# Kernel optimization log

Measured on AMD Instinct MI355X. Metric: run time of the kernel, lower is better.

## Reference

```python
import jax, jax.numpy as jnp
import numpy as np

D = 1024
H = 16
B = 4
L = 1024
EPS = 1e-5


def _ln(x, g, b):
    m = jnp.mean(x, axis=-1, keepdims=True)
    v = jnp.mean((x - m) ** 2, axis=-1, keepdims=True)
    return (x - m) / jnp.sqrt(v + EPS) * g + b


def _bn_eval(x, g, b, mean, var):
    # x: [B, L, C]; per-channel batchnorm in eval mode
    return (x - mean) / jnp.sqrt(var + EPS) * g + b


def setup_inputs() -> dict:
    key = jax.random.key(0)
    ks = jax.random.split(key, 16)
    s = 0.02
    return {
        "q": jax.random.normal(ks[0], (B, L, D), jnp.float32),
        "wq": jax.random.normal(ks[1], (D, D), jnp.float32) * s,
        "bq": jax.random.normal(ks[2], (D,), jnp.float32) * s,
        "wk": jax.random.normal(ks[3], (D, D), jnp.float32) * s,
        "bk": jax.random.normal(ks[4], (D,), jnp.float32) * s,
        "wv": jax.random.normal(ks[5], (D, D), jnp.float32) * s,
        "bv": jax.random.normal(ks[6], (D,), jnp.float32) * s,
        "wo": jax.random.normal(ks[7], (D, D), jnp.float32) * s,
        "bo": jax.random.normal(ks[8], (D,), jnp.float32) * s,
        "w1": jax.random.normal(ks[9], (4 * D, D), jnp.float32) * s,
        "bn1_g": jax.random.uniform(ks[10], (4 * D,), jnp.float32, 0.5, 1.5),
        "bn1_b": jax.random.normal(ks[11], (4 * D,), jnp.float32) * s,
        "bn1_m": jax.random.normal(ks[12], (4 * D,), jnp.float32) * s,
        "bn1_v": jax.random.uniform(ks[13], (4 * D,), jnp.float32, 0.5, 1.5),
        "w2": jax.random.normal(ks[14], (D, 4 * D), jnp.float32) * s,
        "bn2_g": jax.random.uniform(ks[15], (D,), jnp.float32, 0.5, 1.5),
        "bn2_b": jnp.zeros((D,), jnp.float32),
        "bn2_m": jnp.zeros((D,), jnp.float32),
        "bn2_v": jnp.ones((D,), jnp.float32),
        "ln1_g": jnp.ones((D,), jnp.float32),
        "ln1_b": jnp.zeros((D,), jnp.float32),
        "ln3_g": jnp.ones((D,), jnp.float32),
        "ln3_b": jnp.zeros((D,), jnp.float32),
    }


def reference(q, wq, bq, wk, bk, wv, bv, wo, bo,
              w1, bn1_g, bn1_b, bn1_m, bn1_v,
              w2, bn2_g, bn2_b, bn2_m, bn2_v,
              ln1_g, ln1_b, ln3_g, ln3_b):
    hd = D // H
    scale = hd ** -0.5
    # conv1x1 projections == per-token linear: [B,L,D] @ [D,D]^T + bias
    qp = (q @ wq.T + bq).reshape(B, L, H, hd)
    kp = (q @ wk.T + bk).reshape(B, L, H, hd)
    vp = (q @ wv.T + bv).reshape(B, L, H, hd)
    attn = jnp.einsum('blhd,bmhd->bhlm', qp, kp) * scale  # [B,H,L,L]
    attn = jax.nn.softmax(attn, axis=-1)
    out = jnp.einsum('bhlm,bmhd->blhd', attn, vp).reshape(B, L, D)
    out = out @ wo.T + bo
    # post-norm residual block (norm_first=False, use_residual=True)
    x = _ln(q + out, ln1_g, ln1_b)
    # conv-MLP: 1x1 conv -> BN(eval) -> GELU(exact) -> 1x1 conv -> BN(eval)
    h = x @ w1.T                                   # [B,L,4D]
    h = jax.nn.gelu(_bn_eval(h, bn1_g, bn1_b, bn1_m, bn1_v), approximate=False)
    h = _bn_eval(h @ w2.T, bn2_g, bn2_b, bn2_m, bn2_v)  # [B,L,D]
    x = _ln(x + h, ln3_g, ln3_b)
    return x
```

## Files before the change

### kernel.cpp

```cpp
#include <hip/hip_runtime.h>
#include <math.h>

#define EPS 1e-5f

typedef unsigned short ushort_t;
typedef __attribute__((ext_vector_type(8))) __bf16 bf16x8;
typedef __attribute__((ext_vector_type(4))) __bf16 bf16x4;
typedef __attribute__((ext_vector_type(4))) float f32x4;

#define MFMA16(a, b, c) __builtin_amdgcn_mfma_f32_16x16x32_bf16(a, b, c, 0, 0, 0)

#define QSCALE2 0.18033688011112042f

__device__ __forceinline__ unsigned short f2bf(float f) {
  unsigned u = __float_as_uint(f);
  u += 0x7fffu + ((u >> 16) & 1u);
  return (unsigned short)(u >> 16);
}

__device__ __forceinline__ void gload16(const void* g, void* l) {
  __builtin_amdgcn_global_load_lds(
      (__attribute__((address_space(1))) void*)(g),
      (__attribute__((address_space(3))) void*)(l), 16, 0, 0);
}

__global__ __launch_bounds__(256) void cast_all_k(
    const float* __restrict__ wq, const float* __restrict__ wk,
    const float* __restrict__ wv, const float* __restrict__ wo,
    const float* __restrict__ w1, const float* __restrict__ w2,
    const float* __restrict__ q, ushort_t* __restrict__ wqkv,
    ushort_t* __restrict__ wob, ushort_t* __restrict__ w1b,
    ushort_t* __restrict__ w2b, ushort_t* __restrict__ qbf) {
  const int b = blockIdx.x;
  const float* src;
  ushort_t* dst;
  int idx;
  if (b < 2048) {
    const int s = b >> 9;
    src = (s == 0) ? wq : (s == 1) ? wk : (s == 2) ? wv : wo;
    dst = (s == 3) ? wob : wqkv + s * 1048576;
    idx = (b & 511) * 2048 + threadIdx.x * 8;
  } else if (b < 4096) {
    src = w1; dst = w1b; idx = (b - 2048) * 2048 + threadIdx.x * 8;
  } else if (b < 6144) {
    src = w2; dst = w2b; idx = (b - 4096) * 2048 + threadIdx.x * 8;
  } else {
    src = q; dst = qbf; idx = (b - 6144) * 2048 + threadIdx.x * 8;
  }
  float4 a = *(const float4*)(src + idx);
  float4 c = *(const float4*)(src + idx + 4);
  uint4 u;
  u.x = (unsigned)f2bf(a.x) | ((unsigned)f2bf(a.y) << 16);
  u.y = (unsigned)f2bf(a.z) | ((unsigned)f2bf(a.w) << 16);
  u.z = (unsigned)f2bf(c.x) | ((unsigned)f2bf(c.y) << 16);
  u.w = (unsigned)f2bf(c.z) | ((unsigned)f2bf(c.w) << 16);
  *(uint4*)(dst + idx) = u;
}

__global__ __launch_bounds__(256) void bnparam_k(
    const float* __restrict__ g1, const float* __restrict__ b1,
    const float* __restrict__ m1, const float* __restrict__ v1,
    const float* __restrict__ g2, const float* __restrict__ b2,
    const float* __restrict__ m2, const float* __restrict__ v2,
    float* __restrict__ sc1, float* __restrict__ sh1,
    float* __restrict__ sc2, float* __restrict__ sh2) {
  int i = blockIdx.x * 256 + threadIdx.x;
  if (i < 4096) {
    float s = g1[i] * rsqrtf(v1[i] + EPS);
    sc1[i] = s;
    sh1[i] = b1[i] - m1[i] * s;
  } else if (i < 5120) {
    int j = i - 4096;
    float s = g2[j] * rsqrtf(v2[j] + EPS);
    sc2[j] = s;
    sh2[j] = b2[j] - m2[j] * s;
  }
}

template <int KDIM, int EPI, int TM, int TN, int GX, int GY>
__global__ __launch_bounds__(256) void gemm_bt(const ushort_t* __restrict__ A,
                                               const ushort_t* __restrict__ W,
                                               const float* __restrict__ p0,
                                               const float* __restrict__ p1,
                                               const float* __restrict__ p2,
                                               float* __restrict__ outF,
                                               ushort_t* __restrict__ outB) {
  constexpr int BM = 32 * TM, BN = 32 * TN;
  constexpr int LDS_STAGE = (BM + BN) * 64 * 2;
  constexpr int LDS_TR = (EPI == 0) ? 128 * 136 * 2 : 0;
  __shared__ alignas(16) char pool[(LDS_STAGE > LDS_TR) ? LDS_STAGE : LDS_TR];
  ushort_t* As = (ushort_t*)pool;
  ushort_t* Bs = As + BM * 64;

  constexpr int NWG = GX * GY;
  const int id = blockIdx.x;
  const int pos = (id & 7) * (NWG / 8) + (id >> 3);
  const int grp = pos / (8 * GX);
  const int rem = pos % (8 * GX);
  const int by = grp * 8 + (rem & 7);
  const int bx = rem >> 3;
  const int bm = by * BM, bn = bx * BN;

  const int tid = threadIdx.x;
  const int lane = tid & 63;
  const int wid = tid >> 6;
  const int wr = wid >> 1, wc = wid & 1;
  const int fr = lane & 15;
  const int kg = lane >> 4;

  f32x4 acc[TM][TN];
#pragma unroll
  for (int i = 0; i < TM; ++i)
#pragma unroll
    for (int j = 0; j < TN; ++j)
#pragma unroll
      for (int r = 0; r < 4; ++r) acc[i][j][r] = 0.f;

  for (int k0 = 0; k0 < KDIM; k0 += 64) {
#pragma unroll
    for (int p = 0; p < TM; ++p) {
      const int flat = p * 256 + tid;
      const int row = flat >> 3;
      const int gl = (flat & 7) ^ (row & 7);
      gload16(A + (size_t)(bm + row) * KDIM + k0 + gl * 8,
              ((char*)As) + (p * 256 + wid * 64) * 16);
    }
#pragma unroll
    for (int p = 0; p < TN; ++p) {
      const int flat = p * 256 + tid;
      const int row = flat >> 3;
      const int gl = (flat & 7) ^ (row & 7);
      gload16(W + (size_t)(bn + row) * KDIM + k0 + gl * 8,
              ((char*)Bs) + (p * 256 + wid * 64) * 16);
    }
    __syncthreads();
#pragma unroll
    for (int s = 0; s < 2; ++s) {
      bf16x8 af[TM], bfv[TN];
#pragma unroll
      for (int mf = 0; mf < TM; ++mf) {
        const int row = wr * (16 * TM) + mf * 16 + fr;
        const int gl = s * 4 + kg;
        af[mf] = *(const bf16x8*)(((const char*)As) + row * 128 + ((gl ^ (row & 7)) * 16));
      }
#pragma unroll
      for (int nf = 0; nf < TN; ++nf) {
        const int row = wc * (16 * TN) + nf * 16 + fr;
        const int gl = s * 4 + kg;
        bfv[nf] = *(const bf16x8*)(((const char*)Bs) + row * 128 + ((gl ^ (row & 7)) * 16));
      }
#pragma unroll
      for (int mf = 0; mf < TM; ++mf)
#pragma unroll
        for (int nf = 0; nf < TN; ++nf) acc[mf][nf] = MFMA16(af[mf], bfv[nf], acc[mf][nf]);
    }
    __syncthreads();
  }

  if constexpr (EPI == 0) {
    if (bn < 2048) {
#pragma unroll
      for (int mf = 0; mf < TM; ++mf) {
#pragma unroll
        for (int nf = 0; nf < TN; ++nf) {
#pragma unroll
          for (int r = 0; r < 4; ++r) {
            const int m = bm + wr * 64 + mf * 16 + kg * 4 + r;
            const int n = bn + wc * 64 + nf * 16 + fr;
            const int sel = n >> 10;
            const int nl = n & 1023;
            float v = acc[mf][nf][r] + ((sel == 0) ? p0[nl] : p1[nl]);
            if (sel == 0) v *= QSCALE2;
            const int b_ = m >> 10, tok = m & 1023;
            const int h_ = nl >> 6, d_ = nl & 63;
            outB[(size_t)sel * 4194304 + (((size_t)(b_ * 16 + h_) * 1024 + tok) * 64 + d_)] =
                f2bf(v);
          }
        }
      }
    } else {
      __syncthreads();
      ushort_t* T = (ushort_t*)pool;
#pragma unroll
      for (int mf = 0; mf < TM; ++mf) {
#pragma unroll
        for (int nf = 0; nf < TN; ++nf) {
          const int ml = wr * 64 + mf * 16 + kg * 4;
          const int nl = wc * 64 + nf * 16 + fr;
          const float bias = p2[(bn & 1023) + nl];
          bf16x4 pw;
#pragma unroll
          for (int r = 0; r < 4; ++r) pw[r] = (__bf16)(acc[mf][nf][r] + bias);
          *(bf16x4*)(T + nl * 136 + ml) = pw;
        }
      }
      __syncthreads();
      const int b_ = bm >> 10;
      const int tokb = bm & 1023;
#pragma unroll
      for (int it = 0; it < 8; ++it) {
        const int g = it * 256 + tid;
        const int nl = g >> 4;
        const int m0 = (g & 15) * 8;
        bf16x8 v = *(const bf16x8*)(T + nl * 136 + m0);
        const int nloc = (bn - 2048) + nl;
        const int h_ = nloc >> 6, d_ = nloc & 63;
        *(bf16x8*)(outB + 8388608 + (((size_t)(b_ * 16 + h_) * 64 + d_) << 10) + tokb + m0) = v;
      }
    }
  } else {
#pragma unroll
    for (int mf = 0; mf < TM; ++mf) {
#pragma unroll
      for (int nf = 0; nf < TN; ++nf) {
#pragma unroll
        for (int r = 0; r < 4; ++r) {
          const int m = bm + wr * (16 * TM) + mf * 16 + kg * 4 + r;
          const int n = bn + wc * (16 * TN) + nf * 16 + fr;
          float v = acc[mf][nf][r];
          if constexpr (EPI == 1) {
            v += p0[n] + p1[(size_t)m * 1024 + n];
            outF[(size_t)m * 1024 + n] = v;
          } else if constexpr (EPI == 2) {
            float t = v * p0[n] + p1[n];
            float ge = 0.5f * t * (1.f + erff(t * 0.70710678118654752f));
            outB[(size_t)m * 4096 + n] = f2bf(ge);
          } else {
            outF[(size_t)m * 1024 + n] = v * p0[n] + p1[n];
          }
        }
      }
    }
  }
}

__global__ __launch_bounds__(512) void attn_k(const ushort_t* __restrict__ qp,
                                              const ushort_t* __restrict__ kp,
                                              const ushort_t* __restrict__ vt,
                                              ushort_t* __restrict__ aout) {
  __shared__ ushort_t Kt[2][4096];
  __shared__ ushort_t Vt[2][4096];
  __shared__ ushort_t P[8][16][72];
  const int tid = threadIdx.x;
  const int lane = tid & 63;
  const int wid = tid >> 6;
  const int fr = lane & 15;
  const int kg = lane >> 4;
  const int id = blockIdx.x;
  const int slot = id >> 3;
  const int bh = ((id & 7) << 3) | (slot >> 3);
  const int qc = slot & 7;
  const int b_ = bh >> 4, h_ = bh & 15;

  const size_t base = (size_t)bh << 10;
  const int qrow = qc * 128 + wid * 16 + fr;
  bf16x8 qf0 = *(const bf16x8*)(qp + ((base + qrow) << 6) + kg * 8);
  bf16x8 qf1 = *(const bf16x8*)(qp + ((base + qrow) << 6) + 32 + kg * 8);

  const int srow = tid >> 3;
  const int sg16 = ((tid & 7) ^ (srow & 7)) * 16;
  const char* kTileB = (const char*)kp + ((size_t)bh << 17);
  const char* vTileB = (const char*)vt + ((size_t)bh << 17);
  const size_t koff = (size_t)srow * 128 + sg16;
  const size_t voff = (size_t)srow * 2048 + sg16;

#define STAGE(bufi, kt_)                                                      \
  do {                                                                        \
    gload16(kTileB + (size_t)(kt_)*8192 + koff, (char*)Kt[bufi] + wid * 1024); \
    gload16(vTileB + (size_t)(kt_)*128 + voff, (char*)Vt[bufi] + wid * 1024);  \
  } while (0)

  f32x4 oacc[4];
#pragma unroll
  for (int d = 0; d < 4; ++d)
#pragma unroll
    for (int r = 0; r < 4; ++r) oacc[d][r] = 0.f;
  float mrun = -3.0e38f, lrun = 0.f;

  STAGE(0, 0);
  __syncthreads();

  for (int kt = 0; kt < 16; ++kt) {
    const int c = kt & 1;
    if (kt < 15) STAGE(c ^ 1, kt + 1);
    const char* Kc = (const char*)Kt[c];
    const char* Vc = (const char*)Vt[c];

    f32x4 sacc[4];
#pragma unroll
    for (int nf = 0; nf < 4; ++nf)
#pragma unroll
      for (int r = 0; r < 4; ++r) sacc[nf][r] = 0.f;
    __builtin_amdgcn_s_setprio(1);
#pragma unroll
    for (int nf = 0; nf < 4; ++nf) {
      const int r_ = nf * 16 + fr;
      const char* kr = Kc + r_ * 128;
      bf16x8 kf0 = *(const bf16x8*)(kr + ((kg ^ (r_ & 7)) * 16));
      bf16x8 kf1 = *(const bf16x8*)(kr + (((kg + 4) ^ (r_ & 7)) * 16));
      sacc[nf] = MFMA16(kf0, qf0, sacc[nf]);
      sacc[nf] = MFMA16(kf1, qf1, sacc[nf]);
    }
    __builtin_amdgcn_s_setprio(0);
    float mx = sacc[0][0];
#pragma unroll
    for (int nf = 0; nf < 4; ++nf)
#pragma unroll
      for (int r = 0; r < 4; ++r) mx = fmaxf(mx, sacc[nf][r]);
    mx = fmaxf(mx, __shfl_xor(mx, 16));
    mx = fmaxf(mx, __shfl_xor(mx, 32));
    const float mn = fmaxf(mrun, mx);
    const float c_ = exp2f(mrun - mn);
    float rs = 0.f;
#pragma unroll
    for (int nf = 0; nf < 4; ++nf) {
      bf16x4 pw;
#pragma unroll
      for (int r = 0; r < 4; ++r) {
        float ev = exp2f(sacc[nf][r] - mn);
        rs += ev;
        pw[r] = (__bf16)ev;
      }
      *(bf16x4*)(&P[wid][fr][nf * 16 + kg * 4]) = pw;
    }
    rs += __shfl_xor(rs, 16);
    rs += __shfl_xor(rs, 32);
    lrun = lrun * c_ + rs;
    mrun = mn;
    float cb[4];
#pragma unroll
    for (int r = 0; r < 4; ++r) cb[r] = __shfl(c_, kg * 4 + r);
#pragma unroll
    for (int d = 0; d < 4; ++d)
#pragma unroll
      for (int r = 0; r < 4; ++r) oacc[d][r] *= cb[r];
    bf16x8 pa0 = *(const bf16x8*)(&P[wid][fr][kg * 8]);
    bf16x8 pa1 = *(const bf16x8*)(&P[wid][fr][32 + kg * 8]);
    __builtin_amdgcn_s_setprio(1);
#pragma unroll
    for (int df = 0; df < 4; ++df) {
      const int r_ = df * 16 + fr;
      const char* vr_ = Vc + r_ * 128;
      bf16x8 vf0 = *(const bf16x8*)(vr_ + ((kg ^ (r_ & 7)) * 16));
      bf16x8 vf1 = *(const bf16x8*)(vr_ + (((kg + 4) ^ (r_ & 7)) * 16));
      oacc[df] = MFMA16(pa0, vf0, oacc[df]);
      oacc[df] = MFMA16(pa1, vf1, oacc[df]);
    }
    __builtin_amdgcn_s_setprio(0);
    __syncthreads();
  }
#undef STAGE

  float linv[4];
#pragma unroll
  for (int r = 0; r < 4; ++r) linv[r] = 1.f / __shfl(lrun, kg * 4 + r);
#pragma unroll
  for (int df = 0; df < 4; ++df) {
#pragma unroll
    for (int r = 0; r < 4; ++r) {
      const int tok = qc * 128 + wid * 16 + kg * 4 + r;
      const int d_ = df * 16 + fr;
      aout[((size_t)(b_ * 1024 + tok) * 16 + h_) * 64 + d_] = f2bf(oacc[df][r] * linv[r]);
    }
  }
}

template <int MODE>
__global__ __launch_bounds__(256) void ln_k(const float* __restrict__ in1,
                                            const float* __restrict__ in2,
                                            const float* __restrict__ g,
                                            const float* __restrict__ bt,
                                            float* __restrict__ outF,
                                            ushort_t* __restrict__ outB) {
  const int row = blockIdx.x;
  const int tid = threadIdx.x;
  const size_t off = (size_t)row * 1024 + tid * 4;
  float4 v = *(const float4*)(in1 + off);
  if (MODE == 1) {
    float4 u = *(const float4*)(in2 + off);
    v.x += u.x; v.y += u.y; v.z += u.z; v.w += u.w;
  }
  float s = v.x + v.y + v.z + v.w;
  float q = v.x * v.x + v.y * v.y + v.z * v.z + v.w * v.w;
#pragma unroll
  for (int o = 32; o > 0; o >>= 1) {
    s += __shfl_down(s, o);
    q += __shfl_down(q, o);
  }
  __shared__ float rs[4], rq[4], stat[2];
  const int wid = tid >> 6, lane = tid & 63;
  if (lane == 0) { rs[wid] = s; rq[wid] = q; }
  __syncthreads();
  if (tid == 0) {
    float S = rs[0] + rs[1] + rs[2] + rs[3];
    float Q = rq[0] + rq[1] + rq[2] + rq[3];
    float mean = S * (1.f / 1024.f);
    float var = Q * (1.f / 1024.f) - mean * mean;
    stat[0] = mean;
    stat[1] = rsqrtf(var + EPS);
  }
  __syncthreads();
  const float mean = stat[0], rstd = stat[1];
  const int c = tid * 4;
  float4 o4;
  o4.x = (v.x - mean) * rstd * g[c] + bt[c];
  o4.y = (v.y - mean) * rstd * g[c + 1] + bt[c + 1];
  o4.z = (v.z - mean) * rstd * g[c + 2] + bt[c + 2];
  o4.w = (v.w - mean) * rstd * g[c + 3] + bt[c + 3];
  *(float4*)(outF + off) = o4;
  if (MODE == 0) {
    ushort4 ub;
    ub.x = f2bf(o4.x); ub.y = f2bf(o4.y); ub.z = f2bf(o4.z); ub.w = f2bf(o4.w);
    *(ushort4*)(outB + off) = ub;
  }
}

extern "C" void kernel_launch(void* const* d_in, const int* in_sizes, int n_in,
                              void* d_out, int out_size, void* d_ws, size_t ws_size,
                              hipStream_t stream) {
  const float* q    = (const float*)d_in[0];
  const float* wq   = (const float*)d_in[1];
  const float* bq   = (const float*)d_in[2];
  const float* wk   = (const float*)d_in[3];
  const float* bk   = (const float*)d_in[4];
  const float* wv   = (const float*)d_in[5];
  const float* bv   = (const float*)d_in[6];
  const float* wo   = (const float*)d_in[7];
  const float* bo   = (const float*)d_in[8];
  const float* w1   = (const float*)d_in[9];
  const float* bn1g = (const float*)d_in[10];
  const float* bn1b = (const float*)d_in[11];
  const float* bn1m = (const float*)d_in[12];
  const float* bn1v = (const float*)d_in[13];
  const float* w2   = (const float*)d_in[14];
  const float* bn2g = (const float*)d_in[15];
  const float* bn2b = (const float*)d_in[16];
  const float* bn2m = (const float*)d_in[17];
  const float* bn2v = (const float*)d_in[18];
  const float* ln1g = (const float*)d_in[19];
  const float* ln1b = (const float*)d_in[20];
  const float* ln3g = (const float*)d_in[21];
  const float* ln3b = (const float*)d_in[22];

  char* ws = (char*)d_ws;
  const size_t MB = 1u << 20;
  ushort_t* wqkv = (ushort_t*)(ws);
  ushort_t* w1b  = (ushort_t*)(ws + 6 * MB);
  ushort_t* w2b  = (ushort_t*)(ws + 14 * MB);
  ushort_t* wob  = (ushort_t*)(ws + 22 * MB);
  float* sc1 = (float*)(ws + 24 * MB);
  float* sh1 = sc1 + 4096;
  float* sc2 = sh1 + 4096;
  float* sh2 = sc2 + 1024;
  ushort_t* qbf  = (ushort_t*)(ws + 25 * MB);
  ushort_t* qp   = (ushort_t*)(ws + 33 * MB);
  ushort_t* aout = (ushort_t*)(ws + 57 * MB);
  ushort_t* xbf  = (ushort_t*)(ws + 65 * MB);
  float*    h2   = (float*)(ws + 73 * MB);
  ushort_t* h1   = (ushort_t*)(ws + 33 * MB);
  float* X = (float*)d_out;

  const int NM = 1024 * 1024;
  cast_all_k<<<8192, 256, 0, stream>>>(wq, wk, wv, wo, w1, w2, q, wqkv, wob, w1b, w2b, qbf);
  bnparam_k<<<20, 256, 0, stream>>>(bn1g, bn1b, bn1m, bn1v, bn2g, bn2b, bn2m, bn2v,
                                    sc1, sh1, sc2, sh2);

  gemm_bt<1024, 0, 4, 4, 24, 32><<<768, 256, 0, stream>>>(qbf, wqkv, bq, bk, bv, nullptr, qp);
  attn_k<<<512, 512, 0, stream>>>(qp, qp + 4 * NM, qp + 8 * NM, aout);
  gemm_bt<1024, 1, 4, 2, 16, 32><<<512, 256, 0, stream>>>(aout, wob, bo, q, nullptr, X, nullptr);
  ln_k<0><<<4096, 256, 0, stream>>>(X, nullptr, ln1g, ln1b, X, xbf);
  gemm_bt<1024, 2, 4, 4, 32, 32><<<1024, 256, 0, stream>>>(xbf, w1b, sc1, sh1, nullptr, nullptr, h1);
  gemm_bt<4096, 3, 4, 2, 16, 32><<<512, 256, 0, stream>>>(h1, w2b, sc2, sh2, nullptr, h2, nullptr);
  ln_k<1><<<4096, 256, 0, stream>>>(X, h2, ln3g, ln3b, X, nullptr);
}
```

Measured before the change: 242.8 us.

## Double-buffer GEMM LDS loads, generalize warp tiling, use tanh-form GELU

```diff
diff --git a/kernel.cpp b/kernel.cpp
--- a/kernel.cpp
+++ b/kernel.cpp
@@ -77,20 +77,20 @@
   }
 }
 
-template <int KDIM, int EPI, int TM, int TN, int GX, int GY>
-__global__ __launch_bounds__(256) void gemm_bt(const ushort_t* __restrict__ A,
-                                               const ushort_t* __restrict__ W,
-                                               const float* __restrict__ p0,
-                                               const float* __restrict__ p1,
-                                               const float* __restrict__ p2,
-                                               float* __restrict__ outF,
-                                               ushort_t* __restrict__ outB) {
-  constexpr int BM = 32 * TM, BN = 32 * TN;
-  constexpr int LDS_STAGE = (BM + BN) * 64 * 2;
+template <int KDIM, int EPI, int TM, int TN, int WM, int WN, int NTHR, int GX, int GY>
+__global__ __launch_bounds__(NTHR, 2) void gemm_bt(const ushort_t* __restrict__ A,
+                                                   const ushort_t* __restrict__ W,
+                                                   const float* __restrict__ p0,
+                                                   const float* __restrict__ p1,
+                                                   const float* __restrict__ p2,
+                                                   float* __restrict__ outF,
+                                                   ushort_t* __restrict__ outB) {
+  constexpr int BM = 16 * TM * WM, BN = 16 * TN * WN;
+  constexpr int LDS_STAGE = 2 * (BM + BN) * 128;
   constexpr int LDS_TR = (EPI == 0) ? 128 * 136 * 2 : 0;
   __shared__ alignas(16) char pool[(LDS_STAGE > LDS_TR) ? LDS_STAGE : LDS_TR];
-  ushort_t* As = (ushort_t*)pool;
-  ushort_t* Bs = As + BM * 64;
+  constexpr int LA = BM * 8 / NTHR;
+  constexpr int LB = BN * 8 / NTHR;
 
   constexpr int NWG = GX * GY;
   const int id = blockIdx.x;
@@ -104,10 +104,35 @@
   const int tid = threadIdx.x;
   const int lane = tid & 63;
   const int wid = tid >> 6;
-  const int wr = wid >> 1, wc = wid & 1;
+  const int wr = wid / WN, wc = wid % WN;
   const int fr = lane & 15;
   const int kg = lane >> 4;
 
+  const char* Ag0 = (const char*)(A + (size_t)bm * KDIM);
+  const char* Bg0 = (const char*)(W + (size_t)bn * KDIM);
+
+#define STAGE(bufi, t_)                                                        \
+  do {                                                                         \
+    const char* Ag = Ag0 + (size_t)(t_)*128;                                   \
+    const char* Bg = Bg0 + (size_t)(t_)*128;                                   \
+    char* Ab = pool + (bufi) * (BM * 128);                                     \
+    char* Bb = pool + 2 * BM * 128 + (bufi) * (BN * 128);                      \
+    _Pragma("unroll") for (int li = 0; li < LA; ++li) {                        \
+      const int f = li * NTHR + tid;                                           \
+      const int row = f >> 3;                                                  \
+      const int gl = (f & 7) ^ (row & 7);                                      \
+      gload16(Ag + (size_t)row * (KDIM * 2) + gl * 16,                         \
+              Ab + (li * NTHR + wid * 64) * 16);                               \
+    }                                                                          \
+    _Pragma("unroll") for (int li = 0; li < LB; ++li) {                        \
+      const int f = li * NTHR + tid;                                           \
+      const int row = f >> 3;                                                  \
+      const int gl = (f & 7) ^ (row & 7);                                      \
+      gload16(Bg + (size_t)row * (KDIM * 2) + gl * 16,                         \
+              Bb + (li * NTHR + wid * 64) * 16);                               \
+    }                                                                          \
+  } while (0)
+
   f32x4 acc[TM][TN];
 #pragma unroll
   for (int i = 0; i < TM; ++i)
@@ -116,46 +141,36 @@
 #pragma unroll
       for (int r = 0; r < 4; ++r) acc[i][j][r] = 0.f;
 
-  for (int k0 = 0; k0 < KDIM; k0 += 64) {
-#pragma unroll
-    for (int p = 0; p < TM; ++p) {
-      const int flat = p * 256 + tid;
-      const int row = flat >> 3;
-      const int gl = (flat & 7) ^ (row & 7);
-      gload16(A + (size_t)(bm + row) * KDIM + k0 + gl * 8,
-              ((char*)As) + (p * 256 + wid * 64) * 16);
-    }
-#pragma unroll
-    for (int p = 0; p < TN; ++p) {
-      const int flat = p * 256 + tid;
-      const int row = flat >> 3;
-      const int gl = (flat & 7) ^ (row & 7);
-      gload16(W + (size_t)(bn + row) * KDIM + k0 + gl * 8,
-              ((char*)Bs) + (p * 256 + wid * 64) * 16);
-    }
-    __syncthreads();
+  STAGE(0, 0);
+  asm volatile("s_waitcnt vmcnt(0)" ::: "memory");
+  __builtin_amdgcn_s_barrier();
+
+  constexpr int NT = KDIM / 64;
+  for (int t = 0; t < NT; ++t) {
+    const int b = t & 1;
+    if (t + 1 < NT) STAGE(b ^ 1, t + 1);
+    const char* Ac = pool + b * (BM * 128);
+    const char* Bc = pool + 2 * BM * 128 + b * (BN * 128);
 #pragma unroll
     for (int s = 0; s < 2; ++s) {
-      bf16x8 af[TM], bfv[TN];
+      bf16x8 bfv[TN];
+#pragma unroll
+      for (int nf = 0; nf < TN; ++nf) {
+        const int row = wc * (16 * TN) + nf * 16 + fr;
+        bfv[nf] = *(const bf16x8*)(Bc + row * 128 + (((s * 4 + kg) ^ (row & 7)) * 16));
+      }
 #pragma unroll
       for (int mf = 0; mf < TM; ++mf) {
         const int row = wr * (16 * TM) + mf * 16 + fr;
-        const int gl = s * 4 + kg;
-        af[mf] = *(const bf16x8*)(((const char*)As) + row * 128 + ((gl ^ (row & 7)) * 16));
-      }
-#pragma unroll
-      for (int nf = 0; nf < TN; ++nf) {
-        const int row = wc * (16 * TN) + nf * 16 + fr;
-        const int gl = s * 4 + kg;
-        bfv[nf] = *(const bf16x8*)(((const char*)Bs) + row * 128 + ((gl ^ (row & 7)) * 16));
-      }
-#pragma unroll
-      for (int mf = 0; mf < TM; ++mf)
-#pragma unroll
-        for (int nf = 0; nf < TN; ++nf) acc[mf][nf] = MFMA16(af[mf], bfv[nf], acc[mf][nf]);
-    }
-    __syncthreads();
-  }
+        bf16x8 af = *(const bf16x8*)(Ac + row * 128 + (((s * 4 + kg) ^ (row & 7)) * 16));
+#pragma unroll
+        for (int nf = 0; nf < TN; ++nf) acc[mf][nf] = MFMA16(af, bfv[nf], acc[mf][nf]);
+      }
+    }
+    asm volatile("s_waitcnt vmcnt(0)" ::: "memory");
+    __builtin_amdgcn_s_barrier();
+  }
+#undef STAGE
 
   if constexpr (EPI == 0) {
     if (bn < 2048) {
@@ -165,8 +180,8 @@
         for (int nf = 0; nf < TN; ++nf) {
 #pragma unroll
           for (int r = 0; r < 4; ++r) {
-            const int m = bm + wr * 64 + mf * 16 + kg * 4 + r;
-            const int n = bn + wc * 64 + nf * 16 + fr;
+            const int m = bm + wr * (16 * TM) + mf * 16 + kg * 4 + r;
+            const int n = bn + wc * (16 * TN) + nf * 16 + fr;
             const int sel = n >> 10;
             const int nl = n & 1023;
             float v = acc[mf][nf][r] + ((sel == 0) ? p0[nl] : p1[nl]);
@@ -185,8 +200,8 @@
       for (int mf = 0; mf < TM; ++mf) {
 #pragma unroll
         for (int nf = 0; nf < TN; ++nf) {
-          const int ml = wr * 64 + mf * 16 + kg * 4;
-          const int nl = wc * 64 + nf * 16 + fr;
+          const int ml = wr * (16 * TM) + mf * 16 + kg * 4;
+          const int nl = wc * (16 * TN) + nf * 16 + fr;
           const float bias = p2[(bn & 1023) + nl];
           bf16x4 pw;
 #pragma unroll
@@ -222,8 +237,10 @@
             v += p0[n] + p1[(size_t)m * 1024 + n];
             outF[(size_t)m * 1024 + n] = v;
           } else if constexpr (EPI == 2) {
-            float t = v * p0[n] + p1[n];
-            float ge = 0.5f * t * (1.f + erff(t * 0.70710678118654752f));
+            float tt = v * p0[n] + p1[n];
+            float u = tt * (0.7978845608f + 0.0356774081f * tt * tt);
+            float e = exp2f(u * 2.8853900818f);
+            float ge = tt * (1.f - 1.f / (e + 1.f));
             outB[(size_t)m * 4096 + n] = f2bf(ge);
           } else {
             outF[(size_t)m * 1024 + n] = v * p0[n] + p1[n];
@@ -465,11 +482,15 @@
   bnparam_k<<<20, 256, 0, stream>>>(bn1g, bn1b, bn1m, bn1v, bn2g, bn2b, bn2m, bn2v,
                                     sc1, sh1, sc2, sh2);
 
-  gemm_bt<1024, 0, 4, 4, 24, 32><<<768, 256, 0, stream>>>(qbf, wqkv, bq, bk, bv, nullptr, qp);
+  gemm_bt<1024, 0, 4, 4, 2, 2, 256, 24, 32><<<768, 256, 0, stream>>>(
+      qbf, wqkv, bq, bk, bv, nullptr, qp);
   attn_k<<<512, 512, 0, stream>>>(qp, qp + 4 * NM, qp + 8 * NM, aout);
-  gemm_bt<1024, 1, 4, 2, 16, 32><<<512, 256, 0, stream>>>(aout, wob, bo, q, nullptr, X, nullptr);
+  gemm_bt<1024, 1, 4, 2, 2, 2, 256, 16, 32><<<512, 256, 0, stream>>>(
+      aout, wob, bo, q, nullptr, X, nullptr);
   ln_k<0><<<4096, 256, 0, stream>>>(X, nullptr, ln1g, ln1b, X, xbf);
-  gemm_bt<1024, 2, 4, 4, 32, 32><<<1024, 256, 0, stream>>>(xbf, w1b, sc1, sh1, nullptr, nullptr, h1);
-  gemm_bt<4096, 3, 4, 2, 16, 32><<<512, 256, 0, stream>>>(h1, w2b, sc2, sh2, nullptr, h2, nullptr);
+  gemm_bt<1024, 2, 8, 4, 2, 4, 512, 16, 16><<<256, 512, 0, stream>>>(
+      xbf, w1b, sc1, sh1, nullptr, nullptr, h1);
+  gemm_bt<4096, 3, 4, 2, 2, 2, 256, 16, 32><<<512, 256, 0, stream>>>(
+      h1, w2b, sc2, sh2, nullptr, h2, nullptr);
   ln_k<1><<<4096, 256, 0, stream>>>(X, h2, ln3g, ln3b, X, nullptr);
 }
```

After: 211.4 us. 13.0% less time.
